# Optimization experiments

Measured on AMD Instinct MI355X. Metric: run time of the kernel, lower is better.

Reference implementation:

```python
import jax, jax.numpy as jnp
import numpy as np

T, B, NINP, NHID = 1024, 64, 2048, 2048


def setup_inputs() -> dict:
    key = jax.random.key(0)
    ks = jax.random.split(key, 10)
    s = 0.02  # small init for numerical sanity (torch code used uniform(0,1))
    return {
        "x": jax.random.normal(ks[0], (T, B, NINP), dtype=jnp.float32),
        "hidden": jax.random.normal(ks[1], (B, NHID), dtype=jnp.float32),
        "W_cx": jax.random.normal(ks[2], (NHID, NINP), dtype=jnp.float32) * s,
        "W_ih": jax.random.normal(ks[3], (NHID, NHID), dtype=jnp.float32) * s,
        "W_ix": jax.random.normal(ks[4], (NHID, NINP), dtype=jnp.float32) * s,
        "W_fh": jax.random.normal(ks[5], (NHID, NHID), dtype=jnp.float32) * s,
        "W_fx": jax.random.normal(ks[6], (NHID, NINP), dtype=jnp.float32) * s,
        "b_i": jnp.zeros((NHID,), dtype=jnp.float32),
        "b_f": jnp.zeros((NHID,), dtype=jnp.float32),
    }


def reference(x, hidden, W_cx, W_ih, W_ix, W_fh, W_fx, b_i, b_f):
    # Precompute all input-side projections in big batched GEMMs (same math,
    # hoisted out of the sequential loop).
    content = jnp.einsum('tbi,hi->tbh', x, W_cx)            # [T,B,H]
    ix = jnp.einsum('tbi,hi->tbh', x, W_ix) + b_i            # [T,B,H]
    fx = jnp.einsum('tbi,hi->tbh', x, W_fx) + b_f            # [T,B,H]

    def step(h, inp):
        c_t, ix_t, fx_t = inp
        i_t = jax.nn.sigmoid(h @ W_ih.T + ix_t)
        f_t = jax.nn.sigmoid(h @ W_fh.T + fx_t)
        h_new = jnp.tanh(i_t * c_t + f_t * h)
        return h_new, h_new

    nexth, output = jax.lax.scan(step, hidden, (content, ix, fx))
    return output, nexth
```

## Files before the change

kernel.cpp:

```cpp
#include <hip/hip_runtime.h>
#include <cstdint>
#include <cstddef>

#define T_SEQ 1024
#define BATCH 64
#define NH 2048

typedef _Float16 half8 __attribute__((ext_vector_type(8)));
typedef _Float16 half4 __attribute__((ext_vector_type(4)));
typedef float f32x4 __attribute__((ext_vector_type(4)));
typedef unsigned u32x4 __attribute__((ext_vector_type(4)));

__device__ inline void gload_lds16(const void* g, void* l) {
    __builtin_amdgcn_global_load_lds(
        (const __attribute__((address_space(1))) uint32_t*)g,
        (__attribute__((address_space(3))) uint32_t*)l,
        16, 0, 0);
}

#define LLC_LD16NW(dst, addr)                                                \
    asm volatile("global_load_dwordx4 %0, %1, off sc0 sc1"                   \
                 : "=v"(dst) : "v"(addr))
#define LLC_LD4(dst, addr)                                                   \
    asm volatile("global_load_dword %0, %1, off sc0 sc1\n\ts_waitcnt vmcnt(0)" \
                 : "=v"(dst) : "v"(addr))
#define LLC_ST2(addr, val)                                                   \
    asm volatile("global_store_short %0, %1, off sc0 sc1"                    \
                 :: "v"(addr), "v"(val) : "memory")
#define LLC_ST4(addr, val)                                                   \
    asm volatile("global_store_dword %0, %1, off sc0 sc1"                    \
                 :: "v"(addr), "v"(val) : "memory")
#define LLC_ST16(addr, val)                                                  \
    asm volatile("global_store_dwordx4 %0, %1, off sc0 sc1"                  \
                 :: "v"(addr), "v"(val) : "memory")

__device__ inline void wait_vm0() {
    asm volatile("s_waitcnt vmcnt(0)" ::: "memory");
}

#define CANARY32 0xFFFFFFFFu

__global__ __launch_bounds__(256) void cvt_f32_f16(const float* __restrict__ src,
                                                   _Float16* __restrict__ dst,
                                                   long long n) {
    long long i = ((long long)blockIdx.x * 256 + threadIdx.x) * 4;
    long long stride = (long long)gridDim.x * 256 * 4;
    for (; i < n; i += stride) {
        const float4 v = *(const float4*)(src + i);
        half4 o;
        o[0] = (_Float16)v.x; o[1] = (_Float16)v.y;
        o[2] = (_Float16)v.z; o[3] = (_Float16)v.w;
        *(half4*)(dst + i) = o;
    }
}

__global__ __launch_bounds__(256) void proj_gemm(const _Float16* __restrict__ A,
                                                 const _Float16* __restrict__ B,
                                                 _Float16* __restrict__ C, int M) {
    __shared__ _Float16 As[128][64];
    __shared__ _Float16 Bs[128][64];
    const int NBN = 48;
    const int nbm = M >> 7;
    const int nwg = nbm * NBN;
    const int per = nwg >> 3;
    const int bid = blockIdx.x;
    const int swz = (bid & 7) * per + (bid >> 3);
    const int bm = swz / NBN, bn = swz % NBN;

    const int tid = threadIdx.x;
    const int lane = tid & 63, w = tid >> 6;
    const int wm = w & 1, wn = w >> 1;

    f32x4 acc[4][4] = {};

    const int srow = lane >> 3;
    const int scol = (lane & 7) * 8;

    for (int bk = 0; bk < NH / 64; ++bk) {
#pragma unroll
        for (int i = 0; i < 4; ++i) {
            int r = w * 32 + i * 8;
            const _Float16* gA = A + (size_t)(bm * 128 + r + srow) * NH + bk * 64 + scol;
            gload_lds16(gA, &As[r][0]);
            const _Float16* gB = B + (size_t)(bn * 128 + r + srow) * NH + bk * 64 + scol;
            gload_lds16(gB, &Bs[r][0]);
        }
        __syncthreads();
#pragma unroll
        for (int kk = 0; kk < 2; ++kk) {
            half8 af[4], bf[4];
#pragma unroll
            for (int mi = 0; mi < 4; ++mi)
                af[mi] = *(const half8*)&As[wm * 64 + mi * 16 + (lane & 15)][kk * 32 + (lane >> 4) * 8];
#pragma unroll
            for (int ni = 0; ni < 4; ++ni)
                bf[ni] = *(const half8*)&Bs[wn * 64 + ni * 16 + (lane & 15)][kk * 32 + (lane >> 4) * 8];
#pragma unroll
            for (int mi = 0; mi < 4; ++mi)
#pragma unroll
                for (int ni = 0; ni < 4; ++ni)
                    acc[mi][ni] = __builtin_amdgcn_mfma_f32_16x16x32_f16(af[mi], bf[ni], acc[mi][ni], 0, 0, 0);
        }
        __syncthreads();
    }
#pragma unroll
    for (int mi = 0; mi < 4; ++mi)
#pragma unroll
        for (int ni = 0; ni < 4; ++ni)
#pragma unroll
            for (int r = 0; r < 4; ++r) {
                int m = bm * 128 + wm * 64 + mi * 16 + (lane >> 4) * 4 + r;
                int n = bn * 128 + wn * 64 + ni * 16 + (lane & 15);
                C[(size_t)m * 6144 + n] = (_Float16)acc[mi][ni][r];
            }
}

__global__ __launch_bounds__(512, 1) void scan_kernel(
    const _Float16* __restrict__ proj,
    const _Float16* __restrict__ Wr,
    _Float16* hb0, _Float16* hb1,
    const float* __restrict__ b_i, const float* __restrict__ b_f,
    float* __restrict__ out,
    unsigned* hflags, _Float16* part,
    int t0, int nsteps) {
    extern __shared__ char smem[];
    _Float16* Wlds = (_Float16*)smem;
    char* hstage = smem + 131072;

    const int wg = blockIdx.x;
    const int xcd = wg & 7;
    const int slot = wg >> 3;
    const int g = slot & 1;
    const int rem = slot >> 1;
    const int js = xcd * 4 + (rem & 3);
    const int ks = rem >> 2;
    const int j0g = js * 64;
    const int b0 = g * 32;
    const int k0 = ks * 512;

    const int tid = threadIdx.x;
    const int lane = tid & 63;
    const int w = tid >> 6;
    const int mi = w & 1;
    const int nt = w >> 1;

    unsigned* hflags_g = hflags + g * 32;

    for (int q = 0; q < 16; ++q) {
        int e = q * 512 + tid;
        int le = e & 63;
        int u = (e >> 6) & 15;
        int nte = (e >> 10) & 3;
        int gate = e >> 12;
        const _Float16* src = Wr + ((size_t)gate << 22) +
            (size_t)(j0g + nte * 16 + (le & 15)) * NH + k0 + u * 32 + (le >> 4) * 8;
        *(half8*)(Wlds + (((size_t)(gate * 4 + nte) * 16 + u) * 64 + le) * 8) =
            *(const half8*)src;
    }

    const int jj = j0g + nt * 16 + (lane & 15);
    const float bi_s = b_i[jj];
    const float bf_s = b_f[jj];

    float hprev[4], pc[4], pix[4], pfx[4];
    if (ks == 0) {
        const _Float16* hini = (t0 & 1) ? hb1 : hb0;
#pragma unroll
        for (int r = 0; r < 4; ++r) {
            int b = b0 + mi * 16 + (lane >> 4) * 4 + r;
            unsigned tmp;
            asm volatile("global_load_ushort %0, %1, off sc0 sc1\n\ts_waitcnt vmcnt(0)"
                         : "=v"(tmp) : "v"(hini + (size_t)b * NH + jj));
            hprev[r] = (float)__builtin_bit_cast(_Float16, (unsigned short)tmp);
            size_t pbase = (size_t)b * 6144 + jj;
            pc[r] = (float)proj[pbase];
            pix[r] = (float)proj[pbase + 2048];
            pfx[r] = (float)proj[pbase + 4096];
        }
    }

    __syncthreads();

    for (int s = 0; s < nsteps; ++s) {
        const int t = t0 + s;
        const _Float16* hcur = (t & 1) ? hb1 : hb0;
        _Float16* hnxt = (t & 1) ? hb0 : hb1;
        const unsigned tv = (unsigned)t;

        if (w == 0) {
            const unsigned* fa = hflags_g + ks * 8 + (lane & 7);
            while (true) {
                unsigned v;
                LLC_LD4(v, fa);
                if (__all((int)(v >= tv))) break;
                __builtin_amdgcn_s_sleep(1);
            }
        }
        __syncthreads();

        {
            half8 t0v, t1v, t2v, t3v;
            const _Float16* srcb = hcur + (size_t)(b0 + w * 4) * NH + k0 + lane * 8;
            LLC_LD16NW(t0v, srcb);
            LLC_LD16NW(t1v, srcb + NH);
            LLC_LD16NW(t2v, srcb + 2 * NH);
            LLC_LD16NW(t3v, srcb + 3 * NH);
            wait_vm0();
            __builtin_amdgcn_sched_barrier(0);
            const int r0 = w * 4;
            *(half8*)(hstage + (r0 + 0) * 1024 + ((lane * 16) ^ (((r0 + 0) & 7) << 4))) = t0v;
            *(half8*)(hstage + (r0 + 1) * 1024 + ((lane * 16) ^ (((r0 + 1) & 7) << 4))) = t1v;
            *(half8*)(hstage + (r0 + 2) * 1024 + ((lane * 16) ^ (((r0 + 2) & 7) << 4))) = t2v;
            *(half8*)(hstage + (r0 + 3) * 1024 + ((lane * 16) ^ (((r0 + 3) & 7) << 4))) = t3v;
        }
        __syncthreads();

        f32x4 ci = {}, cf = {};
        {
            const int arow = mi * 16 + (lane & 15);
            const char* abase = hstage + arow * 1024;
            const int axor = (arow & 7) << 4;
            const _Float16* wbi = Wlds + (((size_t)(0 * 4 + nt) * 16) * 64 + lane) * 8;
            const _Float16* wbf = Wlds + (((size_t)(1 * 4 + nt) * 16) * 64 + lane) * 8;
#pragma unroll
            for (int u = 0; u < 16; ++u) {
                half8 a = *(const half8*)(abase + ((u * 64 + (lane >> 4) * 16) ^ axor));
                half8 wi = *(const half8*)(wbi + (size_t)u * 512);
                half8 wf = *(const half8*)(wbf + (size_t)u * 512);
                ci = __builtin_amdgcn_mfma_f32_16x16x32_f16(a, wi, ci, 0, 0, 0);
                cf = __builtin_amdgcn_mfma_f32_16x16x32_f16(a, wf, cf, 0, 0, 0);
            }
        }

        const size_t tilebase = (size_t)(((t & 1) * 2 + g) * 32 + js) * 3;

        if (ks != 0) {
            half8 pk;
#pragma unroll
            for (int r = 0; r < 4; ++r) {
                pk[r] = (_Float16)ci[r];
                pk[4 + r] = (_Float16)cf[r];
            }
            _Float16* pb = part + ((tilebase + (ks - 1)) * 8 + w) * 512 + lane * 8;
            LLC_ST16(pb, pk);
        } else {
            _Float16* s0 = part + ((tilebase + 0) * 8 + w) * 512 + lane * 8;
            _Float16* s1 = part + ((tilebase + 1) * 8 + w) * 512 + lane * 8;
            _Float16* s2 = part + ((tilebase + 2) * 8 + w) * 512 + lane * 8;
            u32x4 q0, q1, q2;
            while (true) {
                LLC_LD16NW(q0, s0);
                LLC_LD16NW(q1, s1);
                LLC_LD16NW(q2, s2);
                wait_vm0();
                __builtin_amdgcn_sched_barrier(0);
                bool ok = (q0[0] != CANARY32) && (q1[0] != CANARY32) && (q2[0] != CANARY32);
                if (__all(ok)) break;
                __builtin_amdgcn_s_sleep(1);
            }
            __builtin_amdgcn_sched_barrier(0);
            u32x4 can;
            can[0] = CANARY32; can[1] = CANARY32; can[2] = CANARY32; can[3] = CANARY32;
            LLC_ST16(s0, can);
            LLC_ST16(s1, can);
            LLC_ST16(s2, can);

            half8 p0 = __builtin_bit_cast(half8, q0);
            half8 p1 = __builtin_bit_cast(half8, q1);
            half8 p2 = __builtin_bit_cast(half8, q2);
#pragma unroll
            for (int r = 0; r < 4; ++r) {
                ci[r] += (float)p0[r] + (float)p1[r] + (float)p2[r];
                cf[r] += (float)p0[4 + r] + (float)p1[4 + r] + (float)p2[4 + r];
            }

            float hn_keep[4];
#pragma unroll
            for (int r = 0; r < 4; ++r) {
                int b = b0 + mi * 16 + (lane >> 4) * 4 + r;
                float iv = 1.0f / (1.0f + __expf(-(ci[r] + pix[r] + bi_s)));
                float fv = 1.0f / (1.0f + __expf(-(cf[r] + pfx[r] + bf_s)));
                float z = iv * pc[r] + fv * hprev[r];
                float hn = 1.0f - 2.0f / (__expf(2.0f * z) + 1.0f);
                hprev[r] = hn;
                hn_keep[r] = hn;
                _Float16 hn16 = (_Float16)hn;
                LLC_ST2(hnxt + (size_t)b * NH + jj, hn16);
            }
            wait_vm0();
            __syncthreads();
            if (tid == 0) LLC_ST4(hflags_g + js, (unsigned)(t + 1));

#pragma unroll
            for (int r = 0; r < 4; ++r) {
                int b = b0 + mi * 16 + (lane >> 4) * 4 + r;
                out[(size_t)t * (BATCH * NH) + (size_t)b * NH + jj] = hn_keep[r];
                if (t == T_SEQ - 1)
                    out[(size_t)T_SEQ * (BATCH * NH) + (size_t)b * NH + jj] = hn_keep[r];
            }
            if (s + 1 < nsteps) {
#pragma unroll
                for (int r = 0; r < 4; ++r) {
                    int b = b0 + mi * 16 + (lane >> 4) * 4 + r;
                    size_t pbase = ((size_t)(s + 1) * 64 + b) * 6144 + jj;
                    pc[r] = (float)proj[pbase];
                    pix[r] = (float)proj[pbase + 2048];
                    pfx[r] = (float)proj[pbase + 4096];
                }
            }
        }
    }
}

extern "C" void kernel_launch(void* const* d_in, const int* in_sizes, int n_in,
                              void* d_out, int out_size, void* d_ws, size_t ws_size,
                              hipStream_t stream) {
    const float* x = (const float*)d_in[0];
    const float* hidden = (const float*)d_in[1];
    const float* W_cx = (const float*)d_in[2];
    const float* W_ih = (const float*)d_in[3];
    const float* W_ix = (const float*)d_in[4];
    const float* W_fh = (const float*)d_in[5];
    const float* W_fx = (const float*)d_in[6];
    const float* b_i = (const float*)d_in[7];
    const float* b_f = (const float*)d_in[8];
    float* out = (float*)d_out;

    char* ws = (char*)d_ws;
    size_t off = 0;
    auto alloc = [&](size_t bytes) {
        char* p = ws + off;
        off += (bytes + 255) & ~(size_t)255;
        return p;
    };
    _Float16* Wp = (_Float16*)alloc((size_t)6144 * NH * 2);
    _Float16* Wr = (_Float16*)alloc((size_t)2 * NH * NH * 2);
    _Float16* hb0 = (_Float16*)alloc((size_t)BATCH * NH * 2);
    _Float16* hb1 = (_Float16*)alloc((size_t)BATCH * NH * 2);
    unsigned* hflags = (unsigned*)alloc(256);
    const size_t part_bytes = (size_t)2 * 2 * 32 * 3 * 8 * 512 * 2;
    _Float16* part = (_Float16*)alloc(part_bytes);
    const size_t fixed = off;

    int chunk = 32;
    for (int c = T_SEQ; c >= 32; c >>= 1) {
        size_t need = fixed + (size_t)c * 64 * NH * 2 + (size_t)c * 64 * 6144 * 2 + 1024;
        if (need <= ws_size) { chunk = c; break; }
    }
    _Float16* xh = (_Float16*)alloc((size_t)chunk * 64 * NH * 2);
    _Float16* proj = (_Float16*)alloc((size_t)chunk * 64 * 6144 * 2);

    hipMemsetAsync(hflags, 0, 256, stream);
    hipMemsetAsync(part, 0xFF, part_bytes, stream);

    const long long wsz = (long long)NH * NH;
    cvt_f32_f16<<<2048, 256, 0, stream>>>(W_cx, Wp, wsz);
    cvt_f32_f16<<<2048, 256, 0, stream>>>(W_ix, Wp + wsz, wsz);
    cvt_f32_f16<<<2048, 256, 0, stream>>>(W_fx, Wp + 2 * wsz, wsz);
    cvt_f32_f16<<<2048, 256, 0, stream>>>(W_ih, Wr, wsz);
    cvt_f32_f16<<<2048, 256, 0, stream>>>(W_fh, Wr + wsz, wsz);
    cvt_f32_f16<<<128, 256, 0, stream>>>(hidden, hb0, (long long)BATCH * NH);

    const int nch = T_SEQ / chunk;
    for (int c = 0; c < nch; ++c) {
        const int t0 = c * chunk;
        const int M = chunk * 64;
        cvt_f32_f16<<<2048, 256, 0, stream>>>(x + (size_t)t0 * 64 * NH, xh, (long long)M * NH);
        proj_gemm<<<dim3((M / 128) * 48), 256, 0, stream>>>(xh, Wp, proj, M);
        scan_kernel<<<256, 512, 163840, stream>>>(proj, Wr, hb0, hb1, b_i, b_f,
                                                  out, hflags, part, t0, chunk);
    }
}
```

Before: 9.870 ms.

## Replace per-step flag synchronization with canary-tagged hidden-state ring buffer

Drops the separate per-slice progress flags and the block-wide barrier before publishing them. The hidden state now lives in a 4-slot ring, and consumers poll the h data itself until no fp16 canary value (0xFFFF) remains. Each producer re-poisons the slot that will be reused two steps later. This removes one flag round-trip and a __syncthreads per step, at the cost of polling wider data. It also assumes a real hidden value never encodes as the 0xFFFF NaN pattern.

New measurement: 12.11 ms. +22.7%, slower.

```diff
diff --git a/kernel.cpp b/kernel.cpp
--- a/kernel.cpp
+++ b/kernel.cpp
@@ -5,6 +5,7 @@
 #define T_SEQ 1024
 #define BATCH 64
 #define NH 2048
+#define HSZ (BATCH * NH)
 
 typedef _Float16 half8 __attribute__((ext_vector_type(8)));
 typedef _Float16 half4 __attribute__((ext_vector_type(4)));
@@ -21,14 +22,8 @@
 #define LLC_LD16NW(dst, addr)                                                \
     asm volatile("global_load_dwordx4 %0, %1, off sc0 sc1"                   \
                  : "=v"(dst) : "v"(addr))
-#define LLC_LD4(dst, addr)                                                   \
-    asm volatile("global_load_dword %0, %1, off sc0 sc1\n\ts_waitcnt vmcnt(0)" \
-                 : "=v"(dst) : "v"(addr))
 #define LLC_ST2(addr, val)                                                   \
     asm volatile("global_store_short %0, %1, off sc0 sc1"                    \
-                 :: "v"(addr), "v"(val) : "memory")
-#define LLC_ST4(addr, val)                                                   \
-    asm volatile("global_store_dword %0, %1, off sc0 sc1"                    \
                  :: "v"(addr), "v"(val) : "memory")
 #define LLC_ST16(addr, val)                                                  \
     asm volatile("global_store_dwordx4 %0, %1, off sc0 sc1"                  \
@@ -39,6 +34,15 @@
 }
 
 #define CANARY32 0xFFFFFFFFu
+#define CANARY16 0xFFFFu
+
+__device__ inline bool no_canary16(const u32x4& q) {
+    bool ok = true;
+#pragma unroll
+    for (int d = 0; d < 4; ++d)
+        ok = ok && ((q[d] & 0xFFFFu) != CANARY16) && ((q[d] >> 16) != CANARY16);
+    return ok;
+}
 
 __global__ __launch_bounds__(256) void cvt_f32_f16(const float* __restrict__ src,
                                                    _Float16* __restrict__ dst,
@@ -118,11 +122,10 @@
 __global__ __launch_bounds__(512, 1) void scan_kernel(
     const _Float16* __restrict__ proj,
     const _Float16* __restrict__ Wr,
-    _Float16* hb0, _Float16* hb1,
+    _Float16* hslab,
     const float* __restrict__ b_i, const float* __restrict__ b_f,
     float* __restrict__ out,
-    unsigned* hflags, _Float16* part,
-    int t0, int nsteps) {
+    _Float16* part, int t0, int nsteps) {
     extern __shared__ char smem[];
     _Float16* Wlds = (_Float16*)smem;
     char* hstage = smem + 131072;
@@ -144,8 +147,6 @@
     const int mi = w & 1;
     const int nt = w >> 1;
 
-    unsigned* hflags_g = hflags + g * 32;
-
     for (int q = 0; q < 16; ++q) {
         int e = q * 512 + tid;
         int le = e & 63;
@@ -164,14 +165,11 @@
 
     float hprev[4], pc[4], pix[4], pfx[4];
     if (ks == 0) {
-        const _Float16* hini = (t0 & 1) ? hb1 : hb0;
+        const _Float16* hini = hslab + (size_t)(t0 & 3) * HSZ;
 #pragma unroll
         for (int r = 0; r < 4; ++r) {
             int b = b0 + mi * 16 + (lane >> 4) * 4 + r;
-            unsigned tmp;
-            asm volatile("global_load_ushort %0, %1, off sc0 sc1\n\ts_waitcnt vmcnt(0)"
-                         : "=v"(tmp) : "v"(hini + (size_t)b * NH + jj));
-            hprev[r] = (float)__builtin_bit_cast(_Float16, (unsigned short)tmp);
+            hprev[r] = (float)hini[(size_t)b * NH + jj];
             size_t pbase = (size_t)b * 6144 + jj;
             pc[r] = (float)proj[pbase];
             pix[r] = (float)proj[pbase + 2048];
@@ -183,35 +181,33 @@
 
     for (int s = 0; s < nsteps; ++s) {
         const int t = t0 + s;
-        const _Float16* hcur = (t & 1) ? hb1 : hb0;
-        _Float16* hnxt = (t & 1) ? hb0 : hb1;
-        const unsigned tv = (unsigned)t;
-
-        if (w == 0) {
-            const unsigned* fa = hflags_g + ks * 8 + (lane & 7);
+        const _Float16* hin = hslab + (size_t)(t & 3) * HSZ;
+        _Float16* hout = hslab + (size_t)((t + 1) & 3) * HSZ;
+        _Float16* hre = hslab + (size_t)((t + 3) & 3) * HSZ;
+
+        __syncthreads();
+
+        {
+            const _Float16* srcb = hin + (size_t)(b0 + w * 4) * NH + k0 + lane * 8;
+            u32x4 q0, q1, q2, q3;
             while (true) {
-                unsigned v;
-                LLC_LD4(v, fa);
-                if (__all((int)(v >= tv))) break;
+                LLC_LD16NW(q0, srcb);
+                LLC_LD16NW(q1, srcb + NH);
+                LLC_LD16NW(q2, srcb + 2 * NH);
+                LLC_LD16NW(q3, srcb + 3 * NH);
+                wait_vm0();
+                __builtin_amdgcn_sched_barrier(0);
+                bool ok = no_canary16(q0) && no_canary16(q1) &&
+                          no_canary16(q2) && no_canary16(q3);
+                if (__all(ok)) break;
                 __builtin_amdgcn_s_sleep(1);
             }
-        }
-        __syncthreads();
-
-        {
-            half8 t0v, t1v, t2v, t3v;
-            const _Float16* srcb = hcur + (size_t)(b0 + w * 4) * NH + k0 + lane * 8;
-            LLC_LD16NW(t0v, srcb);
-            LLC_LD16NW(t1v, srcb + NH);
-            LLC_LD16NW(t2v, srcb + 2 * NH);
-            LLC_LD16NW(t3v, srcb + 3 * NH);
-            wait_vm0();
             __builtin_amdgcn_sched_barrier(0);
             const int r0 = w * 4;
-            *(half8*)(hstage + (r0 + 0) * 1024 + ((lane * 16) ^ (((r0 + 0) & 7) << 4))) = t0v;
-            *(half8*)(hstage + (r0 + 1) * 1024 + ((lane * 16) ^ (((r0 + 1) & 7) << 4))) = t1v;
-            *(half8*)(hstage + (r0 + 2) * 1024 + ((lane * 16) ^ (((r0 + 2) & 7) << 4))) = t2v;
-            *(half8*)(hstage + (r0 + 3) * 1024 + ((lane * 16) ^ (((r0 + 3) & 7) << 4))) = t3v;
+            *(half8*)(hstage + (r0 + 0) * 1024 + ((lane * 16) ^ (((r0 + 0) & 7) << 4))) = __builtin_bit_cast(half8, q0);
+            *(half8*)(hstage + (r0 + 1) * 1024 + ((lane * 16) ^ (((r0 + 1) & 7) << 4))) = __builtin_bit_cast(half8, q1);
+            *(half8*)(hstage + (r0 + 2) * 1024 + ((lane * 16) ^ (((r0 + 2) & 7) << 4))) = __builtin_bit_cast(half8, q2);
+            *(half8*)(hstage + (r0 + 3) * 1024 + ((lane * 16) ^ (((r0 + 3) & 7) << 4))) = __builtin_bit_cast(half8, q3);
         }
         __syncthreads();
 
@@ -254,16 +250,23 @@
                 LLC_LD16NW(q2, s2);
                 wait_vm0();
                 __builtin_amdgcn_sched_barrier(0);
-                bool ok = (q0[0] != CANARY32) && (q1[0] != CANARY32) && (q2[0] != CANARY32);
+                bool ok = no_canary16(q0) && no_canary16(q1) && no_canary16(q2);
                 if (__all(ok)) break;
                 __builtin_amdgcn_s_sleep(1);
             }
             __builtin_amdgcn_sched_barrier(0);
+
             u32x4 can;
             can[0] = CANARY32; can[1] = CANARY32; can[2] = CANARY32; can[3] = CANARY32;
             LLC_ST16(s0, can);
             LLC_ST16(s1, can);
             LLC_ST16(s2, can);
+            const unsigned can16 = CANARY16;
+#pragma unroll
+            for (int r = 0; r < 4; ++r) {
+                int b = b0 + mi * 16 + (lane >> 4) * 4 + r;
+                LLC_ST2(hre + (size_t)b * NH + jj, can16);
+            }
 
             half8 p0 = __builtin_bit_cast(half8, q0);
             half8 p1 = __builtin_bit_cast(half8, q1);
@@ -275,21 +278,25 @@
             }
 
             float hn_keep[4];
-#pragma unroll
-            for (int r = 0; r < 4; ++r) {
-                int b = b0 + mi * 16 + (lane >> 4) * 4 + r;
+            _Float16 hn16[4];
+#pragma unroll
+            for (int r = 0; r < 4; ++r) {
                 float iv = 1.0f / (1.0f + __expf(-(ci[r] + pix[r] + bi_s)));
                 float fv = 1.0f / (1.0f + __expf(-(cf[r] + pfx[r] + bf_s)));
                 float z = iv * pc[r] + fv * hprev[r];
                 float hn = 1.0f - 2.0f / (__expf(2.0f * z) + 1.0f);
                 hprev[r] = hn;
                 hn_keep[r] = hn;
-                _Float16 hn16 = (_Float16)hn;
-                LLC_ST2(hnxt + (size_t)b * NH + jj, hn16);
-            }
+                hn16[r] = (_Float16)hn;
+            }
+
             wait_vm0();
-            __syncthreads();
-            if (tid == 0) LLC_ST4(hflags_g + js, (unsigned)(t + 1));
+
+#pragma unroll
+            for (int r = 0; r < 4; ++r) {
+                int b = b0 + mi * 16 + (lane >> 4) * 4 + r;
+                LLC_ST2(hout + (size_t)b * NH + jj, hn16[r]);
+            }
 
 #pragma unroll
             for (int r = 0; r < 4; ++r) {
@@ -335,9 +342,7 @@
     };
     _Float16* Wp = (_Float16*)alloc((size_t)6144 * NH * 2);
     _Float16* Wr = (_Float16*)alloc((size_t)2 * NH * NH * 2);
-    _Float16* hb0 = (_Float16*)alloc((size_t)BATCH * NH * 2);
-    _Float16* hb1 = (_Float16*)alloc((size_t)BATCH * NH * 2);
-    unsigned* hflags = (unsigned*)alloc(256);
+    _Float16* hslab = (_Float16*)alloc((size_t)4 * HSZ * 2);
     const size_t part_bytes = (size_t)2 * 2 * 32 * 3 * 8 * 512 * 2;
     _Float16* part = (_Float16*)alloc(part_bytes);
     const size_t fixed = off;
@@ -350,7 +355,7 @@
     _Float16* xh = (_Float16*)alloc((size_t)chunk * 64 * NH * 2);
     _Float16* proj = (_Float16*)alloc((size_t)chunk * 64 * 6144 * 2);
 
-    hipMemsetAsync(hflags, 0, 256, stream);
+    hipMemsetAsync(hslab + HSZ, 0xFF, (size_t)3 * HSZ * 2, stream);
     hipMemsetAsync(part, 0xFF, part_bytes, stream);
 
     const long long wsz = (long long)NH * NH;
@@ -359,7 +364,7 @@
     cvt_f32_f16<<<2048, 256, 0, stream>>>(W_fx, Wp + 2 * wsz, wsz);
     cvt_f32_f16<<<2048, 256, 0, stream>>>(W_ih, Wr, wsz);
     cvt_f32_f16<<<2048, 256, 0, stream>>>(W_fh, Wr + wsz, wsz);
-    cvt_f32_f16<<<128, 256, 0, stream>>>(hidden, hb0, (long long)BATCH * NH);
+    cvt_f32_f16<<<128, 256, 0, stream>>>(hidden, hslab, (long long)BATCH * NH);
 
     const int nch = T_SEQ / chunk;
     for (int c = 0; c < nch; ++c) {
@@ -367,7 +372,7 @@
         const int M = chunk * 64;
         cvt_f32_f16<<<2048, 256, 0, stream>>>(x + (size_t)t0 * 64 * NH, xh, (long long)M * NH);
         proj_gemm<<<dim3((M / 128) * 48), 256, 0, stream>>>(xh, Wp, proj, M);
-        scan_kernel<<<256, 512, 163840, stream>>>(proj, Wr, hb0, hb1, b_i, b_f,
-                                                  out, hflags, part, t0, chunk);
-    }
-}
+        scan_kernel<<<256, 512, 163840, stream>>>(proj, Wr, hslab, b_i, b_f,
+                                                  out, part, t0, chunk);
+    }
+}
```
